# Performance work log

Hardware: AMD Instinct MI355X
Metric: run time of the kernel (lower is better)

Reference implementation:

```python
import jax, jax.numpy as jnp
import numpy as np


def _norm(graph):
    # graph: [B, N, N]. Row-normalize: D^{-1} A, with nan/inf -> 0.
    degree = jnp.sum(graph, axis=2)            # [B, N]
    inv = 1.0 / degree
    inv = jnp.where(jnp.isnan(inv) | jnp.isinf(inv), jnp.zeros_like(inv), inv)
    # diag_embed(inv) @ graph == inv[:, :, None] * graph (per-row scale)
    return inv[:, :, None] * graph


def setup_inputs() -> dict:
    key = jax.random.key(0)
    k0, k1 = jax.random.split(key)
    B, N = 16, 1024
    adj0 = jax.random.uniform(k0, (B, N, N), dtype=jnp.float32)
    adj1 = jax.random.uniform(k1, (B, N, N), dtype=jnp.float32)
    return {"adj0": adj0, "adj1": adj1}


def reference(adj0, adj1):
    return (_norm(adj0), _norm(adj1))
```

## Files before the change

### kernel.cpp

```cpp
#include <hip/hip_runtime.h>

#define NCOLS 1024

typedef float vfloat4 __attribute__((ext_vector_type(4)));

__global__ __launch_bounds__(256) void Normalizer_row_kernel(
    const float* __restrict__ a0, const float* __restrict__ a1,
    float* __restrict__ out, int rows_per_input) {
    const int tid  = threadIdx.x;
    const int lane = tid & 63;
    const int wave = tid >> 6;
    const int row  = blockIdx.x * 4 + wave;

    const float* src = (row < rows_per_input)
        ? a0 + (size_t)row * NCOLS
        : a1 + (size_t)(row - rows_per_input) * NCOLS;
    float* dst = out + (size_t)row * NCOLS;

    const vfloat4* src4 = reinterpret_cast<const vfloat4*>(src);
    vfloat4* dst4 = reinterpret_cast<vfloat4*>(dst);

    vfloat4 v0 = __builtin_nontemporal_load(&src4[lane]);
    vfloat4 v1 = __builtin_nontemporal_load(&src4[lane + 64]);
    vfloat4 v2 = __builtin_nontemporal_load(&src4[lane + 128]);
    vfloat4 v3 = __builtin_nontemporal_load(&src4[lane + 192]);

    float s = ((v0.x + v0.y) + (v0.z + v0.w)) + ((v1.x + v1.y) + (v1.z + v1.w))
            + ((v2.x + v2.y) + (v2.z + v2.w)) + ((v3.x + v3.y) + (v3.z + v3.w));
#pragma unroll
    for (int off = 32; off > 0; off >>= 1)
        s += __shfl_xor(s, off, 64);

    float inv = 1.0f / s;
    if (!isfinite(inv)) inv = 0.0f;

    v0 *= inv;
    v1 *= inv;
    v2 *= inv;
    v3 *= inv;

    __builtin_nontemporal_store(v0, &dst4[lane]);
    __builtin_nontemporal_store(v1, &dst4[lane + 64]);
    __builtin_nontemporal_store(v2, &dst4[lane + 128]);
    __builtin_nontemporal_store(v3, &dst4[lane + 192]);
}

extern "C" void kernel_launch(void* const* d_in, const int* in_sizes, int n_in,
                              void* d_out, int out_size, void* d_ws, size_t ws_size,
                              hipStream_t stream) {
    const float* a0 = (const float*)d_in[0];
    const float* a1 = (const float*)d_in[1];
    float* out = (float*)d_out;

    const int rows_per_input = in_sizes[0] / NCOLS;
    const int total_rows = 2 * rows_per_input;
    const int blocks = total_rows / 4;

    Normalizer_row_kernel<<<blocks, 256, 0, stream>>>(a0, a1, out, rows_per_input);
}
```

Measured before the change: 217.8 us.

## Split row normalization into separate sum and scale kernels using workspace

```diff
diff --git a/kernel.cpp b/kernel.cpp
--- a/kernel.cpp
+++ b/kernel.cpp
@@ -4,26 +4,23 @@
 
 typedef float vfloat4 __attribute__((ext_vector_type(4)));
 
-__global__ __launch_bounds__(256) void Normalizer_row_kernel(
+
+__global__ __launch_bounds__(256) void Normalizer_sum_kernel(
     const float* __restrict__ a0, const float* __restrict__ a1,
-    float* __restrict__ out, int rows_per_input) {
-    const int tid  = threadIdx.x;
-    const int lane = tid & 63;
-    const int wave = tid >> 6;
+    float* __restrict__ inv_out, int rows_per_input) {
+    const int lane = threadIdx.x & 63;
+    const int wave = threadIdx.x >> 6;
     const int row  = blockIdx.x * 4 + wave;
 
     const float* src = (row < rows_per_input)
         ? a0 + (size_t)row * NCOLS
         : a1 + (size_t)(row - rows_per_input) * NCOLS;
-    float* dst = out + (size_t)row * NCOLS;
+    const vfloat4* s4 = reinterpret_cast<const vfloat4*>(src);
 
-    const vfloat4* src4 = reinterpret_cast<const vfloat4*>(src);
-    vfloat4* dst4 = reinterpret_cast<vfloat4*>(dst);
-
-    vfloat4 v0 = __builtin_nontemporal_load(&src4[lane]);
-    vfloat4 v1 = __builtin_nontemporal_load(&src4[lane + 64]);
-    vfloat4 v2 = __builtin_nontemporal_load(&src4[lane + 128]);
-    vfloat4 v3 = __builtin_nontemporal_load(&src4[lane + 192]);
+    vfloat4 v0 = s4[lane];
+    vfloat4 v1 = s4[lane + 64];
+    vfloat4 v2 = s4[lane + 128];
+    vfloat4 v3 = s4[lane + 192];
 
     float s = ((v0.x + v0.y) + (v0.z + v0.w)) + ((v1.x + v1.y) + (v1.z + v1.w))
             + ((v2.x + v2.y) + (v2.z + v2.w)) + ((v3.x + v3.y) + (v3.z + v3.w));
@@ -34,15 +31,68 @@
     float inv = 1.0f / s;
     if (!isfinite(inv)) inv = 0.0f;
 
-    v0 *= inv;
-    v1 *= inv;
-    v2 *= inv;
-    v3 *= inv;
+    if (lane == 0) inv_out[row] = inv;
+}
 
-    __builtin_nontemporal_store(v0, &dst4[lane]);
-    __builtin_nontemporal_store(v1, &dst4[lane + 64]);
-    __builtin_nontemporal_store(v2, &dst4[lane + 128]);
-    __builtin_nontemporal_store(v3, &dst4[lane + 192]);
+__global__ __launch_bounds__(256) void Normalizer_scale_kernel(
+    const float* __restrict__ a0, const float* __restrict__ a1,
+    const float* __restrict__ inv_in, float* __restrict__ out,
+    int rows_per_input) {
+    const int lane = threadIdx.x & 63;
+    const int wave = threadIdx.x >> 6;
+    const int row  = blockIdx.x * 4 + wave;
+
+    const float* src = (row < rows_per_input)
+        ? a0 + (size_t)row * NCOLS
+        : a1 + (size_t)(row - rows_per_input) * NCOLS;
+    const vfloat4* s4 = reinterpret_cast<const vfloat4*>(src);
+
+    const float inv = inv_in[row];
+
+    vfloat4 v0 = s4[lane];
+    vfloat4 v1 = s4[lane + 64];
+    vfloat4 v2 = s4[lane + 128];
+    vfloat4 v3 = s4[lane + 192];
+
+    vfloat4* d4 = reinterpret_cast<vfloat4*>(out + (size_t)row * NCOLS);
+    __builtin_nontemporal_store(v0 * inv, &d4[lane]);
+    __builtin_nontemporal_store(v1 * inv, &d4[lane + 64]);
+    __builtin_nontemporal_store(v2 * inv, &d4[lane + 128]);
+    __builtin_nontemporal_store(v3 * inv, &d4[lane + 192]);
+}
+
+__global__ __launch_bounds__(256) void Normalizer_row_kernel(
+    const float* __restrict__ a0, const float* __restrict__ a1,
+    float* __restrict__ out, int rows_per_input) {
+    const int lane = threadIdx.x & 63;
+    const int wave = threadIdx.x >> 6;
+    const int row  = blockIdx.x * 4 + wave;
+
+    const float* src = (row < rows_per_input)
+        ? a0 + (size_t)row * NCOLS
+        : a1 + (size_t)(row - rows_per_input) * NCOLS;
+    const vfloat4* s4 = reinterpret_cast<const vfloat4*>(src);
+    float* dst = out + (size_t)row * NCOLS;
+    vfloat4* d4 = reinterpret_cast<vfloat4*>(dst);
+
+    vfloat4 v0 = __builtin_nontemporal_load(&s4[lane]);
+    vfloat4 v1 = __builtin_nontemporal_load(&s4[lane + 64]);
+    vfloat4 v2 = __builtin_nontemporal_load(&s4[lane + 128]);
+    vfloat4 v3 = __builtin_nontemporal_load(&s4[lane + 192]);
+
+    float s = ((v0.x + v0.y) + (v0.z + v0.w)) + ((v1.x + v1.y) + (v1.z + v1.w))
+            + ((v2.x + v2.y) + (v2.z + v2.w)) + ((v3.x + v3.y) + (v3.z + v3.w));
+#pragma unroll
+    for (int off = 32; off > 0; off >>= 1)
+        s += __shfl_xor(s, off, 64);
+
+    float inv = 1.0f / s;
+    if (!isfinite(inv)) inv = 0.0f;
+
+    __builtin_nontemporal_store(v0 * inv, &d4[lane]);
+    __builtin_nontemporal_store(v1 * inv, &d4[lane + 64]);
+    __builtin_nontemporal_store(v2 * inv, &d4[lane + 128]);
+    __builtin_nontemporal_store(v3 * inv, &d4[lane + 192]);
 }
 
 extern "C" void kernel_launch(void* const* d_in, const int* in_sizes, int n_in,
@@ -56,5 +106,14 @@
     const int total_rows = 2 * rows_per_input;
     const int blocks = total_rows / 4;
 
-    Normalizer_row_kernel<<<blocks, 256, 0, stream>>>(a0, a1, out, rows_per_input);
+    if (d_ws != nullptr && ws_size >= (size_t)total_rows * sizeof(float)) {
+        float* inv_ws = (float*)d_ws;
+        Normalizer_sum_kernel<<<blocks, 256, 0, stream>>>(
+            a0, a1, inv_ws, rows_per_input);
+        Normalizer_scale_kernel<<<blocks, 256, 0, stream>>>(
+            a0, a1, inv_ws, out, rows_per_input);
+    } else {
+        Normalizer_row_kernel<<<blocks, 256, 0, stream>>>(
+            a0, a1, out, rows_per_input);
+    }
 }
```

Result: slower. 244.6 us (+12.3%).
